# Kernel tuning notes

Hardware: AMD Instinct MI355X
Metric: run time of the kernel (lower is better)

## Reference

```python
import jax, jax.numpy as jnp
import numpy as np

NEG_SLOPE = 0.2

def _gat(x_src, x_dst, W_src, W_dst, a_src, a_dst, bias, src, dst, num_dst):
    # Bipartite PyG GATConv, heads=1, concat, add_self_loops=False.
    h_src = x_src @ W_src              # [N_src, H]
    h_dst = x_dst @ W_dst              # [N_dst, H]
    # Per-edge attention logits: leaky_relu(a_src.h_src[i] + a_dst.h_dst[j])
    e = jax.nn.leaky_relu((h_src @ a_src)[src] + (h_dst @ a_dst)[dst], NEG_SLOPE)  # [E]
    # Segment softmax over incoming edges of each dst node
    m = jax.ops.segment_max(e, dst, num_segments=num_dst)
    m = jnp.where(jnp.isfinite(m), m, 0.0)  # empty segments -> safe
    ex = jnp.exp(e - m[dst])
    denom = jax.ops.segment_sum(ex, dst, num_segments=num_dst)
    alpha = ex / denom[dst]            # [E]
    # Scatter-sum weighted source messages
    out = jax.ops.segment_sum(alpha[:, None] * h_src[src], dst, num_segments=num_dst)
    return out + bias


def setup_inputs() -> dict:
    key = jax.random.key(0)
    ks = jax.random.split(key, 20)
    N_L, N_A, D, H, O, E = 100000, 20000, 128, 128, 64, 500000
    s = 1.0 / np.sqrt(D)
    inp = {
        'x_label': jax.random.normal(ks[0], (N_L, D), jnp.float32),
        'x_attr': jax.random.normal(ks[1], (N_A, D), jnp.float32),
        'W_src_la': jax.random.normal(ks[2], (D, H), jnp.float32) * s,
        'W_dst_la': jax.random.normal(ks[3], (D, H), jnp.float32) * s,
        'a_src_la': jax.random.normal(ks[4], (H,), jnp.float32) * s,
        'a_dst_la': jax.random.normal(ks[5], (H,), jnp.float32) * s,
        'b_la': jax.random.normal(ks[6], (H,), jnp.float32) * 0.01,
        'W_src_al': jax.random.normal(ks[7], (D, H), jnp.float32) * s,
        'W_dst_al': jax.random.normal(ks[8], (D, H), jnp.float32) * s,
        'a_src_al': jax.random.normal(ks[9], (H,), jnp.float32) * s,
        'a_dst_al': jax.random.normal(ks[10], (H,), jnp.float32) * s,
        'b_al': jax.random.normal(ks[11], (H,), jnp.float32) * 0.01,
        'W_lin': jax.random.normal(ks[12], (H, O), jnp.float32) * s,
        'b_lin': jax.random.normal(ks[13], (O,), jnp.float32) * 0.01,
        'edge_src_la': jax.random.randint(ks[14], (E,), 0, N_L, jnp.int32),
        'edge_dst_la': jax.random.randint(ks[15], (E,), 0, N_A, jnp.int32),
        'edge_src_al': jax.random.randint(ks[16], (E,), 0, N_A, jnp.int32),
        'edge_dst_al': jax.random.randint(ks[17], (E,), 0, N_L, jnp.int32),
    }
    return inp


def reference(x_label, x_attr, W_src_la, W_dst_la, a_src_la, a_dst_la, b_la,
              W_src_al, W_dst_al, a_src_al, a_dst_al, b_al, W_lin, b_lin,
              edge_src_la, edge_dst_la, edge_src_al, edge_dst_al):
    N_L = x_label.shape[0]
    N_A = x_attr.shape[0]
    # label -> attribute GAT (output for 'attribute' nodes)
    h_attr = _gat(x_label, x_attr, W_src_la, W_dst_la, a_src_la, a_dst_la, b_la,
                  edge_src_la, edge_dst_la, N_A)
    # attribute -> label GAT (output for 'label' nodes)
    h_label = _gat(x_attr, x_label, W_src_al, W_dst_al, a_src_al, a_dst_al, b_al,
                   edge_src_al, edge_dst_al, N_L)
    h_attr = jax.nn.relu(h_attr)  # computed as in original (unused downstream)
    h_label = jax.nn.relu(h_label)
    out = h_label @ W_lin + b_lin
    return out
```

## Files before the change

kernel.cpp:

```cpp
#include <hip/hip_runtime.h>
#include <math.h>

#define NEG_SLOPE 0.2f

typedef __attribute__((ext_vector_type(8))) short bf16x8;
typedef __attribute__((ext_vector_type(4))) float f32x4;

__device__ __forceinline__ unsigned short f2bf(float f) {
    unsigned u = __float_as_uint(f);
    unsigned r = (u + 0x7FFFu + ((u >> 16) & 1u)) >> 16;
    return (unsigned short)r;
}

__device__ __forceinline__ void acc8(float* a, uint4 u, float x) {
    a[0] += x * __uint_as_float(u.x << 16);
    a[1] += x * __uint_as_float(u.x & 0xFFFF0000u);
    a[2] += x * __uint_as_float(u.y << 16);
    a[3] += x * __uint_as_float(u.y & 0xFFFF0000u);
    a[4] += x * __uint_as_float(u.z << 16);
    a[5] += x * __uint_as_float(u.z & 0xFFFF0000u);
    a[6] += x * __uint_as_float(u.w << 16);
    a[7] += x * __uint_as_float(u.w & 0xFFFF0000u);
}

__global__ void k_wvec(const float* __restrict__ Wd, const float* __restrict__ ad,
                       const float* __restrict__ Ws, const float* __restrict__ as_,
                       float* __restrict__ wdst, float* __restrict__ wsrc) {
    int t = threadIdx.x;
    const float* W = (t < 128) ? Wd : Ws;
    const float* a = (t < 128) ? ad : as_;
    int d = t & 127;
    float s = 0.f;
    #pragma unroll 8
    for (int h = 0; h < 128; ++h) s += W[d * 128 + h] * a[h];
    if (t < 128) wdst[d] = s; else wsrc[d] = s;
}

__global__ void k_rowdot(const float* __restrict__ X, const float* __restrict__ v,
                         float* __restrict__ out, int n) {
    int gw = (int)((blockIdx.x * blockDim.x + threadIdx.x) >> 6);
    int lane = threadIdx.x & 63;
    int half = lane >> 5, li = lane & 31;
    int row = gw * 2 + half;
    if (row >= n) return;
    const float4* X4 = (const float4*)X;
    const float4* V4 = (const float4*)v;
    float4 x = X4[(size_t)row * 32 + li];
    float4 b = V4[li];
    float p = x.x * b.x + x.y * b.y + x.z * b.z + x.w * b.w;
    #pragma unroll
    for (int off = 16; off; off >>= 1) p += __shfl_xor(p, off);
    if (li == 0) out[row] = p;
}

__global__ __launch_bounds__(256) void k_hsrc(const float* __restrict__ X,
                                              const float* __restrict__ W,
                                              unsigned short* __restrict__ Hb, int nrows) {
    __shared__ float Xs[32][128];
    int t = threadIdx.x;
    int row0 = blockIdx.x * 32;
    #pragma unroll
    for (int i = 0; i < 16; ++i) {
        int idx = t + i * 256;
        int r = idx >> 7;
        Xs[r][idx & 127] = (row0 + r < nrows) ? X[(size_t)row0 * 128 + idx] : 0.f;
    }
    __syncthreads();
    int cg = t & 31, rg = t >> 5;
    float acc[4][4];
    #pragma unroll
    for (int i = 0; i < 4; ++i)
        #pragma unroll
        for (int j = 0; j < 4; ++j) acc[i][j] = 0.f;
    const float4* W4 = (const float4*)W;
    #pragma unroll 4
    for (int d = 0; d < 128; ++d) {
        float4 wv = W4[d * 32 + cg];
        float x0 = Xs[rg * 4 + 0][d], x1 = Xs[rg * 4 + 1][d];
        float x2 = Xs[rg * 4 + 2][d], x3 = Xs[rg * 4 + 3][d];
        acc[0][0] += x0 * wv.x; acc[0][1] += x0 * wv.y; acc[0][2] += x0 * wv.z; acc[0][3] += x0 * wv.w;
        acc[1][0] += x1 * wv.x; acc[1][1] += x1 * wv.y; acc[1][2] += x1 * wv.z; acc[1][3] += x1 * wv.w;
        acc[2][0] += x2 * wv.x; acc[2][1] += x2 * wv.y; acc[2][2] += x2 * wv.z; acc[2][3] += x2 * wv.w;
        acc[3][0] += x3 * wv.x; acc[3][1] += x3 * wv.y; acc[3][2] += x3 * wv.z; acc[3][3] += x3 * wv.w;
    }
    #pragma unroll
    for (int i = 0; i < 4; ++i) {
        int gr = row0 + rg * 4 + i;
        if (gr < nrows) {
            ushort4 o;
            o.x = f2bf(acc[i][0]); o.y = f2bf(acc[i][1]);
            o.z = f2bf(acc[i][2]); o.w = f2bf(acc[i][3]);
            *(ushort4*)&Hb[(size_t)gr * 128 + cg * 4] = o;
        }
    }
}

__global__ void k_deg(const int* __restrict__ dst, int* __restrict__ deg, int E) {
    int i = blockIdx.x * blockDim.x + threadIdx.x;
    if (i < E) atomicAdd(&deg[dst[i]], 1);
}

__global__ __launch_bounds__(256) void k_scanA(const int* __restrict__ deg,
                                               int* __restrict__ bsum, int n) {
    __shared__ int sd[256];
    int t = threadIdx.x;
    int base = blockIdx.x * 1024 + t * 4;
    int s = 0;
    #pragma unroll
    for (int i = 0; i < 4; ++i) if (base + i < n) s += deg[base + i];
    sd[t] = s;
    __syncthreads();
    for (int off = 128; off; off >>= 1) {
        if (t < off) sd[t] += sd[t + off];
        __syncthreads();
    }
    if (t == 0) bsum[blockIdx.x] = sd[0];
}

__global__ __launch_bounds__(128) void k_scanB(int* __restrict__ bsum, int nb,
                                               int* __restrict__ rowptr, int n, int E) {
    __shared__ int ss[128];
    int t = threadIdx.x;
    if (nb <= 128) {
        int v = (t < nb) ? bsum[t] : 0;
        ss[t] = v;
        __syncthreads();
        for (int off = 1; off < 128; off <<= 1) {
            int u = (t >= off) ? ss[t - off] : 0;
            __syncthreads();
            ss[t] += u;
            __syncthreads();
        }
        if (t < nb) bsum[t] = ss[t] - v;
    } else if (t == 0) {
        int run = 0;
        for (int i = 0; i < nb; ++i) { int v = bsum[i]; bsum[i] = run; run += v; }
    }
    if (t == 0) rowptr[n] = E;
}

__global__ __launch_bounds__(256) void k_scanC(const int* __restrict__ deg,
                                               const int* __restrict__ bsum,
                                               int* __restrict__ rowptr, int n) {
    __shared__ int ss[256];
    int t = threadIdx.x;
    int base = blockIdx.x * 1024 + t * 4;
    int d[4]; int tsum = 0;
    #pragma unroll
    for (int i = 0; i < 4; ++i) { d[i] = (base + i < n) ? deg[base + i] : 0; tsum += d[i]; }
    ss[t] = tsum;
    __syncthreads();
    for (int off = 1; off < 256; off <<= 1) {
        int v = (t >= off) ? ss[t - off] : 0;
        __syncthreads();
        ss[t] += v;
        __syncthreads();
    }
    int excl = ss[t] - tsum + bsum[blockIdx.x];
    #pragma unroll
    for (int i = 0; i < 4; ++i) {
        if (base + i < n) rowptr[base + i] = excl;
        excl += d[i];
    }
}

__global__ void k_scatter(const int* __restrict__ src, const int* __restrict__ dst,
                          const float* __restrict__ ssrc, const float* __restrict__ sdst,
                          const int* __restrict__ rowptr, int* __restrict__ cursor,
                          int2* __restrict__ csr_pair, int E) {
    int i = blockIdx.x * blockDim.x + threadIdx.x;
    if (i >= E) return;
    int s = src[i], d = dst[i];
    float e = ssrc[s] + sdst[d];
    e = e > 0.f ? e : NEG_SLOPE * e;
    float ex = __expf(e);
    int pos = rowptr[d] + atomicAdd(&cursor[d], 1);
    csr_pair[pos] = make_int2(s, __float_as_int(ex));
}

__global__ __launch_bounds__(256) void k_gat(
    const int* __restrict__ rowptr, const int2* __restrict__ csr_pair,
    const unsigned short* __restrict__ Hb, const float* __restrict__ b_al,
    unsigned short* __restrict__ Gb, int n) {
    int t = threadIdx.x;
    int wave = t >> 6, lane = t & 63;
    int grp = lane >> 4, gl = lane & 15;
    int row = blockIdx.x * 16 + wave * 4 + grp;
    if (row >= n) return;
    int beg = rowptr[row], end = rowptr[row + 1];
    const uint4* H16 = (const uint4*)Hb;
    float a[8];
    #pragma unroll
    for (int k = 0; k < 8; ++k) a[k] = 0.f;
    float denom = 0.f;
    int j = beg;
    for (; j + 4 <= end; j += 4) {
        int2 p0 = csr_pair[j], p1 = csr_pair[j + 1];
        int2 p2 = csr_pair[j + 2], p3 = csr_pair[j + 3];
        float x0 = __int_as_float(p0.y), x1 = __int_as_float(p1.y);
        float x2 = __int_as_float(p2.y), x3 = __int_as_float(p3.y);
        uint4 u0 = H16[(size_t)p0.x * 16 + gl];
        uint4 u1 = H16[(size_t)p1.x * 16 + gl];
        uint4 u2 = H16[(size_t)p2.x * 16 + gl];
        uint4 u3 = H16[(size_t)p3.x * 16 + gl];
        denom += (x0 + x1) + (x2 + x3);
        acc8(a, u0, x0); acc8(a, u1, x1); acc8(a, u2, x2); acc8(a, u3, x3);
    }
    for (; j + 2 <= end; j += 2) {
        int2 p0 = csr_pair[j], p1 = csr_pair[j + 1];
        float x0 = __int_as_float(p0.y), x1 = __int_as_float(p1.y);
        uint4 u0 = H16[(size_t)p0.x * 16 + gl];
        uint4 u1 = H16[(size_t)p1.x * 16 + gl];
        denom += x0 + x1;
        acc8(a, u0, x0); acc8(a, u1, x1);
    }
    if (j < end) {
        int2 p0 = csr_pair[j];
        float x0 = __int_as_float(p0.y);
        uint4 u0 = H16[(size_t)p0.x * 16 + gl];
        denom += x0;
        acc8(a, u0, x0);
    }
    float inv = denom > 0.f ? 1.f / denom : 0.f;
    const float4* B4 = (const float4*)b_al;
    float4 bA = B4[gl * 2], bB = B4[gl * 2 + 1];
    ushort4 ga, gb;
    ga.x = f2bf(fmaxf(a[0] * inv + bA.x, 0.f)); ga.y = f2bf(fmaxf(a[1] * inv + bA.y, 0.f));
    ga.z = f2bf(fmaxf(a[2] * inv + bA.z, 0.f)); ga.w = f2bf(fmaxf(a[3] * inv + bA.w, 0.f));
    gb.x = f2bf(fmaxf(a[4] * inv + bB.x, 0.f)); gb.y = f2bf(fmaxf(a[5] * inv + bB.y, 0.f));
    gb.z = f2bf(fmaxf(a[6] * inv + bB.z, 0.f)); gb.w = f2bf(fmaxf(a[7] * inv + bB.w, 0.f));
    unsigned short* Gr = Gb + (size_t)row * 128 + gl * 8;
    *(ushort4*)Gr = ga;
    *(ushort4*)(Gr + 4) = gb;
}

__global__ void k_wconv(const float* __restrict__ Wlin, unsigned short* __restrict__ Wb) {
    int idx = blockIdx.x * 256 + threadIdx.x;
    int col = idx >> 7, k = idx & 127;
    Wb[idx] = f2bf(Wlin[k * 64 + col]);
}

__global__ __launch_bounds__(256) void k_out_mfma(
    const unsigned short* __restrict__ Gb, const unsigned short* __restrict__ Wb,
    const float* __restrict__ b_lin, float* __restrict__ out, int n) {
    int t = threadIdx.x;
    int wave = t >> 6, lane = t & 63;
    int m = lane & 15, kq = lane >> 4;
    int row0 = blockIdx.x * 64 + wave * 16;
    int ra = row0 + m;
    if (ra >= n) ra = n - 1;
    const bf16x8* A = (const bf16x8*)(Gb + (size_t)ra * 128);
    f32x4 acc0 = {0.f, 0.f, 0.f, 0.f};
    f32x4 acc1 = {0.f, 0.f, 0.f, 0.f};
    f32x4 acc2 = {0.f, 0.f, 0.f, 0.f};
    f32x4 acc3 = {0.f, 0.f, 0.f, 0.f};
    const bf16x8* B0 = (const bf16x8*)(Wb + (size_t)(0 * 16 + m) * 128);
    const bf16x8* B1 = (const bf16x8*)(Wb + (size_t)(1 * 16 + m) * 128);
    const bf16x8* B2 = (const bf16x8*)(Wb + (size_t)(2 * 16 + m) * 128);
    const bf16x8* B3 = (const bf16x8*)(Wb + (size_t)(3 * 16 + m) * 128);
    #pragma unroll
    for (int s = 0; s < 4; ++s) {
        int ci = s * 4 + kq;
        bf16x8 a = A[ci];
        acc0 = __builtin_amdgcn_mfma_f32_16x16x32_bf16(a, B0[ci], acc0, 0, 0, 0);
        acc1 = __builtin_amdgcn_mfma_f32_16x16x32_bf16(a, B1[ci], acc1, 0, 0, 0);
        acc2 = __builtin_amdgcn_mfma_f32_16x16x32_bf16(a, B2[ci], acc2, 0, 0, 0);
        acc3 = __builtin_amdgcn_mfma_f32_16x16x32_bf16(a, B3[ci], acc3, 0, 0, 0);
    }
    float bl0 = b_lin[0 * 16 + m], bl1 = b_lin[1 * 16 + m];
    float bl2 = b_lin[2 * 16 + m], bl3 = b_lin[3 * 16 + m];
    #pragma unroll
    for (int j = 0; j < 4; ++j) {
        int row = row0 + kq * 4 + j;
        if (row < n) {
            float* orow = out + (size_t)row * 64;
            orow[0 * 16 + m] = acc0[j] + bl0;
            orow[1 * 16 + m] = acc1[j] + bl1;
            orow[2 * 16 + m] = acc2[j] + bl2;
            orow[3 * 16 + m] = acc3[j] + bl3;
        }
    }
}

extern "C" void kernel_launch(void* const* d_in, const int* in_sizes, int n_in,
                              void* d_out, int out_size, void* d_ws, size_t ws_size,
                              hipStream_t stream) {
    const float* x_label  = (const float*)d_in[0];
    const float* x_attr   = (const float*)d_in[1];
    const float* W_src_al = (const float*)d_in[7];
    const float* W_dst_al = (const float*)d_in[8];
    const float* a_src_al = (const float*)d_in[9];
    const float* a_dst_al = (const float*)d_in[10];
    const float* b_al     = (const float*)d_in[11];
    const float* W_lin    = (const float*)d_in[12];
    const float* b_lin    = (const float*)d_in[13];
    const int* edge_src   = (const int*)d_in[16];
    const int* edge_dst   = (const int*)d_in[17];

    const int D = 128;
    const int N_L = in_sizes[0] / D;
    const int N_A = in_sizes[1] / D;
    const int E   = in_sizes[16];
    const int nb  = (N_L + 1023) / 1024;

    float* ws = (float*)d_ws;
    float* s_src = ws;
    float* s_dst = s_src + N_A;
    float* wdst  = s_dst + N_L;
    float* wsrc  = wdst + 128;
    int*   deg    = (int*)(wsrc + 128);
    int*   cursor = deg + N_L;
    int*   rowptr = cursor + N_L;
    int*   bsum   = rowptr + N_L + 4;
    int2*  csr_pair = (int2*)(bsum + 128);
    unsigned short* Hb = (unsigned short*)(csr_pair + E);
    unsigned short* Gb = Hb + (size_t)N_A * 128;
    unsigned short* Wb = Gb + (size_t)(N_L + 64) * 128;
    float* out = (float*)d_out;

    hipMemsetAsync(deg, 0, (size_t)2 * N_L * sizeof(int), stream);

    k_wvec<<<1, 256, 0, stream>>>(W_dst_al, a_dst_al, W_src_al, a_src_al, wdst, wsrc);
    k_rowdot<<<(N_L + 7) / 8, 256, 0, stream>>>(x_label, wdst, s_dst, N_L);
    k_rowdot<<<(N_A + 7) / 8, 256, 0, stream>>>(x_attr, wsrc, s_src, N_A);
    k_wconv<<<32, 256, 0, stream>>>(W_lin, Wb);
    k_hsrc<<<(N_A + 31) / 32, 256, 0, stream>>>(x_attr, W_src_al, Hb, N_A);
    k_deg<<<(E + 255) / 256, 256, 0, stream>>>(edge_dst, deg, E);
    k_scanA<<<nb, 256, 0, stream>>>(deg, bsum, N_L);
    k_scanB<<<1, 128, 0, stream>>>(bsum, nb, rowptr, N_L, E);
    k_scanC<<<nb, 256, 0, stream>>>(deg, bsum, rowptr, N_L);
    k_scatter<<<(E + 255) / 256, 256, 0, stream>>>(edge_src, edge_dst, s_src, s_dst,
                                                   rowptr, cursor, csr_pair, E);
    k_gat<<<(N_L + 15) / 16, 256, 0, stream>>>(rowptr, csr_pair, Hb, b_al, Gb, N_L);
    k_out_mfma<<<(N_L + 63) / 64, 256, 0, stream>>>(Gb, Wb, b_lin, out, N_L);
}
```

Measured before the change: 258.5 us.

## Merge independent launches into role-dispatched kernels and fuse GAT with output GEMM

Independent preprocessing steps are packed into two multi-role kernels. The first handles degree counting, the attention weight vectors and the W_lin bf16 conversion. The second handles the block scan, both row-dot products and the H_src projection. The GAT aggregation is fused with the output MFMA GEMM, so aggregated rows are staged in XOR-swizzled shared memory instead of being written to and reread from a global bf16 buffer. This cuts launch count and global traffic, but the fused kernel uses 16KB of LDS per block and has fewer blocks, each processing 4 rows per group serially, which may reduce the latency hiding for the gathers.

```diff
diff --git a/kernel.cpp b/kernel.cpp
--- a/kernel.cpp
+++ b/kernel.cpp
@@ -23,23 +23,41 @@
     a[7] += x * __uint_as_float(u.w & 0xFFFF0000u);
 }
 
-__global__ void k_wvec(const float* __restrict__ Wd, const float* __restrict__ ad,
-                       const float* __restrict__ Ws, const float* __restrict__ as_,
-                       float* __restrict__ wdst, float* __restrict__ wsrc) {
-    int t = threadIdx.x;
-    const float* W = (t < 128) ? Wd : Ws;
-    const float* a = (t < 128) ? ad : as_;
-    int d = t & 127;
-    float s = 0.f;
-    #pragma unroll 8
-    for (int h = 0; h < 128; ++h) s += W[d * 128 + h] * a[h];
-    if (t < 128) wdst[d] = s; else wsrc[d] = s;
-}
-
-__global__ void k_rowdot(const float* __restrict__ X, const float* __restrict__ v,
-                         float* __restrict__ out, int n) {
-    int gw = (int)((blockIdx.x * blockDim.x + threadIdx.x) >> 6);
-    int lane = threadIdx.x & 63;
+__device__ __forceinline__ unsigned pack2(unsigned short lo, unsigned short hi) {
+    return (unsigned)lo | ((unsigned)hi << 16);
+}
+
+__global__ __launch_bounds__(256) void k_pre(
+    const int* __restrict__ dst, int* __restrict__ deg, int E, int nbDeg,
+    const float* __restrict__ Wd, const float* __restrict__ ad,
+    const float* __restrict__ Ws, const float* __restrict__ as_,
+    float* __restrict__ wdst, float* __restrict__ wsrc,
+    const float* __restrict__ Wlin, unsigned short* __restrict__ Wb) {
+    int b = blockIdx.x, t = threadIdx.x;
+    if (b < nbDeg) {
+        int i = b * 256 + t;
+        if (i < E) atomicAdd(&deg[dst[i]], 1);
+    } else if (b == nbDeg) {
+        const float* W = (t < 128) ? Wd : Ws;
+        const float* a = (t < 128) ? ad : as_;
+        int d = t & 127;
+        float s = 0.f;
+        #pragma unroll 8
+        for (int h = 0; h < 128; ++h) s += W[d * 128 + h] * a[h];
+        if (t < 128) wdst[d] = s; else wsrc[d] = s;
+    } else {
+        int idx = (b - nbDeg - 1) * 256 + t;
+        int col = idx >> 7, k = idx & 127;
+        Wb[idx] = f2bf(Wlin[k * 64 + col]);
+    }
+}
+
+__device__ __forceinline__ void rowdot_role(const float* __restrict__ X,
+                                            const float* __restrict__ v,
+                                            float* __restrict__ out, int n,
+                                            int vb, int t) {
+    int gw = vb * 4 + (t >> 6);
+    int lane = t & 63;
     int half = lane >> 5, li = lane & 31;
     int row = gw * 2 + half;
     if (row >= n) return;
@@ -53,17 +71,16 @@
     if (li == 0) out[row] = p;
 }
 
-__global__ __launch_bounds__(256) void k_hsrc(const float* __restrict__ X,
-                                              const float* __restrict__ W,
-                                              unsigned short* __restrict__ Hb, int nrows) {
-    __shared__ float Xs[32][128];
-    int t = threadIdx.x;
-    int row0 = blockIdx.x * 32;
+__device__ __forceinline__ void hsrc_role(const float* __restrict__ X,
+                                          const float* __restrict__ W,
+                                          unsigned short* __restrict__ Hb,
+                                          int nrows, int row0, int t,
+                                          float* __restrict__ Xs ) {
     #pragma unroll
     for (int i = 0; i < 16; ++i) {
         int idx = t + i * 256;
         int r = idx >> 7;
-        Xs[r][idx & 127] = (row0 + r < nrows) ? X[(size_t)row0 * 128 + idx] : 0.f;
+        Xs[r * 128 + (idx & 127)] = (row0 + r < nrows) ? X[(size_t)row0 * 128 + idx] : 0.f;
     }
     __syncthreads();
     int cg = t & 31, rg = t >> 5;
@@ -76,8 +93,8 @@
     #pragma unroll 4
     for (int d = 0; d < 128; ++d) {
         float4 wv = W4[d * 32 + cg];
-        float x0 = Xs[rg * 4 + 0][d], x1 = Xs[rg * 4 + 1][d];
-        float x2 = Xs[rg * 4 + 2][d], x3 = Xs[rg * 4 + 3][d];
+        float x0 = Xs[(rg * 4 + 0) * 128 + d], x1 = Xs[(rg * 4 + 1) * 128 + d];
+        float x2 = Xs[(rg * 4 + 2) * 128 + d], x3 = Xs[(rg * 4 + 3) * 128 + d];
         acc[0][0] += x0 * wv.x; acc[0][1] += x0 * wv.y; acc[0][2] += x0 * wv.z; acc[0][3] += x0 * wv.w;
         acc[1][0] += x1 * wv.x; acc[1][1] += x1 * wv.y; acc[1][2] += x1 * wv.z; acc[1][3] += x1 * wv.w;
         acc[2][0] += x2 * wv.x; acc[2][1] += x2 * wv.y; acc[2][2] += x2 * wv.z; acc[2][3] += x2 * wv.w;
@@ -95,26 +112,35 @@
     }
 }
 
-__global__ void k_deg(const int* __restrict__ dst, int* __restrict__ deg, int E) {
-    int i = blockIdx.x * blockDim.x + threadIdx.x;
-    if (i < E) atomicAdd(&deg[dst[i]], 1);
-}
-
-__global__ __launch_bounds__(256) void k_scanA(const int* __restrict__ deg,
-                                               int* __restrict__ bsum, int n) {
-    __shared__ int sd[256];
-    int t = threadIdx.x;
-    int base = blockIdx.x * 1024 + t * 4;
-    int s = 0;
-    #pragma unroll
-    for (int i = 0; i < 4; ++i) if (base + i < n) s += deg[base + i];
-    sd[t] = s;
-    __syncthreads();
-    for (int off = 128; off; off >>= 1) {
-        if (t < off) sd[t] += sd[t + off];
+__global__ __launch_bounds__(256) void k_mid(
+    const int* __restrict__ deg, int* __restrict__ bsum, int nScan, int n,
+    const float* __restrict__ xL, const float* __restrict__ wdst,
+    float* __restrict__ sdst, int nRL, int NL,
+    const float* __restrict__ xA, const float* __restrict__ wsrc,
+    float* __restrict__ ssrc, int nRA, int NA,
+    const float* __restrict__ Wsrc, unsigned short* __restrict__ Hb) {
+    __shared__ float smemf[32 * 128];
+    int b = blockIdx.x, t = threadIdx.x;
+    if (b < nScan) {
+        int* sd = (int*)smemf;
+        int base = b * 1024 + t * 4;
+        int s = 0;
+        #pragma unroll
+        for (int i = 0; i < 4; ++i) if (base + i < n) s += deg[base + i];
+        sd[t] = s;
         __syncthreads();
-    }
-    if (t == 0) bsum[blockIdx.x] = sd[0];
+        for (int off = 128; off; off >>= 1) {
+            if (t < off) sd[t] += sd[t + off];
+            __syncthreads();
+        }
+        if (t == 0) bsum[b] = sd[0];
+    } else if (b < nScan + nRL) {
+        rowdot_role(xL, wdst, sdst, NL, b - nScan, t);
+    } else if (b < nScan + nRL + nRA) {
+        rowdot_role(xA, wsrc, ssrc, NA, b - nScan - nRL, t);
+    } else {
+        hsrc_role(xA, Wsrc, Hb, NA, (b - nScan - nRL - nRA) * 32, t, smemf);
+    }
 }
 
 __global__ __launch_bounds__(128) void k_scanB(int* __restrict__ bsum, int nb,
@@ -178,78 +204,77 @@
     csr_pair[pos] = make_int2(s, __float_as_int(ex));
 }
 
-__global__ __launch_bounds__(256) void k_gat(
+__global__ __launch_bounds__(256) void k_gatout(
     const int* __restrict__ rowptr, const int2* __restrict__ csr_pair,
     const unsigned short* __restrict__ Hb, const float* __restrict__ b_al,
-    unsigned short* __restrict__ Gb, int n) {
+    const unsigned short* __restrict__ Wb, const float* __restrict__ b_lin,
+    float* __restrict__ out, int n) {
+    __shared__ unsigned short Gs[64 * 128];
     int t = threadIdx.x;
     int wave = t >> 6, lane = t & 63;
     int grp = lane >> 4, gl = lane & 15;
-    int row = blockIdx.x * 16 + wave * 4 + grp;
-    if (row >= n) return;
-    int beg = rowptr[row], end = rowptr[row + 1];
     const uint4* H16 = (const uint4*)Hb;
-    float a[8];
-    #pragma unroll
-    for (int k = 0; k < 8; ++k) a[k] = 0.f;
-    float denom = 0.f;
-    int j = beg;
-    for (; j + 4 <= end; j += 4) {
-        int2 p0 = csr_pair[j], p1 = csr_pair[j + 1];
-        int2 p2 = csr_pair[j + 2], p3 = csr_pair[j + 3];
-        float x0 = __int_as_float(p0.y), x1 = __int_as_float(p1.y);
-        float x2 = __int_as_float(p2.y), x3 = __int_as_float(p3.y);
-        uint4 u0 = H16[(size_t)p0.x * 16 + gl];
-        uint4 u1 = H16[(size_t)p1.x * 16 + gl];
-        uint4 u2 = H16[(size_t)p2.x * 16 + gl];
-        uint4 u3 = H16[(size_t)p3.x * 16 + gl];
-        denom += (x0 + x1) + (x2 + x3);
-        acc8(a, u0, x0); acc8(a, u1, x1); acc8(a, u2, x2); acc8(a, u3, x3);
-    }
-    for (; j + 2 <= end; j += 2) {
-        int2 p0 = csr_pair[j], p1 = csr_pair[j + 1];
-        float x0 = __int_as_float(p0.y), x1 = __int_as_float(p1.y);
-        uint4 u0 = H16[(size_t)p0.x * 16 + gl];
-        uint4 u1 = H16[(size_t)p1.x * 16 + gl];
-        denom += x0 + x1;
-        acc8(a, u0, x0); acc8(a, u1, x1);
-    }
-    if (j < end) {
-        int2 p0 = csr_pair[j];
-        float x0 = __int_as_float(p0.y);
-        uint4 u0 = H16[(size_t)p0.x * 16 + gl];
-        denom += x0;
-        acc8(a, u0, x0);
-    }
-    float inv = denom > 0.f ? 1.f / denom : 0.f;
+    int row0b = blockIdx.x * 64;
     const float4* B4 = (const float4*)b_al;
     float4 bA = B4[gl * 2], bB = B4[gl * 2 + 1];
-    ushort4 ga, gb;
-    ga.x = f2bf(fmaxf(a[0] * inv + bA.x, 0.f)); ga.y = f2bf(fmaxf(a[1] * inv + bA.y, 0.f));
-    ga.z = f2bf(fmaxf(a[2] * inv + bA.z, 0.f)); ga.w = f2bf(fmaxf(a[3] * inv + bA.w, 0.f));
-    gb.x = f2bf(fmaxf(a[4] * inv + bB.x, 0.f)); gb.y = f2bf(fmaxf(a[5] * inv + bB.y, 0.f));
-    gb.z = f2bf(fmaxf(a[6] * inv + bB.z, 0.f)); gb.w = f2bf(fmaxf(a[7] * inv + bB.w, 0.f));
-    unsigned short* Gr = Gb + (size_t)row * 128 + gl * 8;
-    *(ushort4*)Gr = ga;
-    *(ushort4*)(Gr + 4) = gb;
-}
-
-__global__ void k_wconv(const float* __restrict__ Wlin, unsigned short* __restrict__ Wb) {
-    int idx = blockIdx.x * 256 + threadIdx.x;
-    int col = idx >> 7, k = idx & 127;
-    Wb[idx] = f2bf(Wlin[k * 64 + col]);
-}
-
-__global__ __launch_bounds__(256) void k_out_mfma(
-    const unsigned short* __restrict__ Gb, const unsigned short* __restrict__ Wb,
-    const float* __restrict__ b_lin, float* __restrict__ out, int n) {
-    int t = threadIdx.x;
-    int wave = t >> 6, lane = t & 63;
+
+    #pragma unroll
+    for (int rr = 0; rr < 4; ++rr) {
+        int rl = wave * 16 + rr * 4 + grp;
+        int row = row0b + rl;
+        uint4 gpack = make_uint4(0u, 0u, 0u, 0u);
+        if (row < n) {
+            int beg = rowptr[row], end = rowptr[row + 1];
+            float a[8];
+            #pragma unroll
+            for (int k = 0; k < 8; ++k) a[k] = 0.f;
+            float denom = 0.f;
+            int j = beg;
+            for (; j + 4 <= end; j += 4) {
+                int2 p0 = csr_pair[j], p1 = csr_pair[j + 1];
+                int2 p2 = csr_pair[j + 2], p3 = csr_pair[j + 3];
+                float x0 = __int_as_float(p0.y), x1 = __int_as_float(p1.y);
+                float x2 = __int_as_float(p2.y), x3 = __int_as_float(p3.y);
+                uint4 u0 = H16[(size_t)p0.x * 16 + gl];
+                uint4 u1 = H16[(size_t)p1.x * 16 + gl];
+                uint4 u2 = H16[(size_t)p2.x * 16 + gl];
+                uint4 u3 = H16[(size_t)p3.x * 16 + gl];
+                denom += (x0 + x1) + (x2 + x3);
+                acc8(a, u0, x0); acc8(a, u1, x1); acc8(a, u2, x2); acc8(a, u3, x3);
+            }
+            for (; j + 2 <= end; j += 2) {
+                int2 p0 = csr_pair[j], p1 = csr_pair[j + 1];
+                float x0 = __int_as_float(p0.y), x1 = __int_as_float(p1.y);
+                uint4 u0 = H16[(size_t)p0.x * 16 + gl];
+                uint4 u1 = H16[(size_t)p1.x * 16 + gl];
+                denom += x0 + x1;
+                acc8(a, u0, x0); acc8(a, u1, x1);
+            }
+            if (j < end) {
+                int2 p0 = csr_pair[j];
+                float x0 = __int_as_float(p0.y);
+                uint4 u0 = H16[(size_t)p0.x * 16 + gl];
+                denom += x0;
+                acc8(a, u0, x0);
+            }
+            float inv = denom > 0.f ? 1.f / denom : 0.f;
+            unsigned short g0 = f2bf(fmaxf(a[0] * inv + bA.x, 0.f));
+            unsigned short g1 = f2bf(fmaxf(a[1] * inv + bA.y, 0.f));
+            unsigned short g2 = f2bf(fmaxf(a[2] * inv + bA.z, 0.f));
+            unsigned short g3 = f2bf(fmaxf(a[3] * inv + bA.w, 0.f));
+            unsigned short g4 = f2bf(fmaxf(a[4] * inv + bB.x, 0.f));
+            unsigned short g5 = f2bf(fmaxf(a[5] * inv + bB.y, 0.f));
+            unsigned short g6 = f2bf(fmaxf(a[6] * inv + bB.z, 0.f));
+            unsigned short g7 = f2bf(fmaxf(a[7] * inv + bB.w, 0.f));
+            gpack = make_uint4(pack2(g0, g1), pack2(g2, g3), pack2(g4, g5), pack2(g6, g7));
+        }
+        int slot = gl ^ (rl & 15);
+        *(uint4*)&Gs[rl * 128 + slot * 8] = gpack;
+    }
+    __syncthreads();
+
     int m = lane & 15, kq = lane >> 4;
-    int row0 = blockIdx.x * 64 + wave * 16;
-    int ra = row0 + m;
-    if (ra >= n) ra = n - 1;
-    const bf16x8* A = (const bf16x8*)(Gb + (size_t)ra * 128);
+    int rl = wave * 16 + m;
     f32x4 acc0 = {0.f, 0.f, 0.f, 0.f};
     f32x4 acc1 = {0.f, 0.f, 0.f, 0.f};
     f32x4 acc2 = {0.f, 0.f, 0.f, 0.f};
@@ -261,7 +286,8 @@
     #pragma unroll
     for (int s = 0; s < 4; ++s) {
         int ci = s * 4 + kq;
-        bf16x8 a = A[ci];
+        int slot = ci ^ m;
+        bf16x8 a = *(const bf16x8*)&Gs[rl * 128 + slot * 8];
         acc0 = __builtin_amdgcn_mfma_f32_16x16x32_bf16(a, B0[ci], acc0, 0, 0, 0);
         acc1 = __builtin_amdgcn_mfma_f32_16x16x32_bf16(a, B1[ci], acc1, 0, 0, 0);
         acc2 = __builtin_amdgcn_mfma_f32_16x16x32_bf16(a, B2[ci], acc2, 0, 0, 0);
@@ -269,6 +295,7 @@
     }
     float bl0 = b_lin[0 * 16 + m], bl1 = b_lin[1 * 16 + m];
     float bl2 = b_lin[2 * 16 + m], bl3 = b_lin[3 * 16 + m];
+    int row0 = row0b + wave * 16;
     #pragma unroll
     for (int j = 0; j < 4; ++j) {
         int row = row0 + kq * 4 + j;
@@ -301,7 +328,12 @@
     const int N_L = in_sizes[0] / D;
     const int N_A = in_sizes[1] / D;
     const int E   = in_sizes[16];
-    const int nb  = (N_L + 1023) / 1024;
+
+    const int nbDeg = (E + 255) / 256;
+    const int nScan = (N_L + 1023) / 1024;
+    const int nRL   = (N_L + 7) / 8;
+    const int nRA   = (N_A + 7) / 8;
+    const int nH    = (N_A + 31) / 32;
 
     float* ws = (float*)d_ws;
     float* s_src = ws;
@@ -310,27 +342,28 @@
     float* wsrc  = wdst + 128;
     int*   deg    = (int*)(wsrc + 128);
     int*   cursor = deg + N_L;
-    int*   rowptr = cursor + N_L;
-    int*   bsum   = rowptr + N_L + 4;
-    int2*  csr_pair = (int2*)(bsum + 128);
+    int*   bsum   = cursor + N_L;
+    int*   rowptr = bsum + 128;
+    int2*  csr_pair = (int2*)(rowptr + N_L + 4);
     unsigned short* Hb = (unsigned short*)(csr_pair + E);
-    unsigned short* Gb = Hb + (size_t)N_A * 128;
-    unsigned short* Wb = Gb + (size_t)(N_L + 64) * 128;
+    unsigned short* Wb = Hb + (size_t)N_A * 128;
+
     float* out = (float*)d_out;
 
     hipMemsetAsync(deg, 0, (size_t)2 * N_L * sizeof(int), stream);
 
-    k_wvec<<<1, 256, 0, stream>>>(W_dst_al, a_dst_al, W_src_al, a_src_al, wdst, wsrc);
-    k_rowdot<<<(N_L + 7) / 8, 256, 0, stream>>>(x_label, wdst, s_dst, N_L);
-    k_rowdot<<<(N_A + 7) / 8, 256, 0, stream>>>(x_attr, wsrc, s_src, N_A);
-    k_wconv<<<32, 256, 0, stream>>>(W_lin, Wb);
-    k_hsrc<<<(N_A + 31) / 32, 256, 0, stream>>>(x_attr, W_src_al, Hb, N_A);
-    k_deg<<<(E + 255) / 256, 256, 0, stream>>>(edge_dst, deg, E);
-    k_scanA<<<nb, 256, 0, stream>>>(deg, bsum, N_L);
-    k_scanB<<<1, 128, 0, stream>>>(bsum, nb, rowptr, N_L, E);
-    k_scanC<<<nb, 256, 0, stream>>>(deg, bsum, rowptr, N_L);
-    k_scatter<<<(E + 255) / 256, 256, 0, stream>>>(edge_src, edge_dst, s_src, s_dst,
-                                                   rowptr, cursor, csr_pair, E);
-    k_gat<<<(N_L + 15) / 16, 256, 0, stream>>>(rowptr, csr_pair, Hb, b_al, Gb, N_L);
-    k_out_mfma<<<(N_L + 63) / 64, 256, 0, stream>>>(Gb, Wb, b_lin, out, N_L);
-}
+    k_pre<<<nbDeg + 1 + 32, 256, 0, stream>>>(edge_dst, deg, E, nbDeg,
+                                              W_dst_al, a_dst_al, W_src_al, a_src_al,
+                                              wdst, wsrc, W_lin, Wb);
+    k_mid<<<nScan + nRL + nRA + nH, 256, 0, stream>>>(
+        deg, bsum, nScan, N_L,
+        x_label, wdst, s_dst, nRL, N_L,
+        x_attr, wsrc, s_src, nRA, N_A,
+        W_src_al, Hb);
+    k_scanB<<<1, 128, 0, stream>>>(bsum, nScan, rowptr, N_L, E);
+    k_scanC<<<nScan, 256, 0, stream>>>(deg, bsum, rowptr, N_L);
+    k_scatter<<<nbDeg, 256, 0, stream>>>(edge_src, edge_dst, s_src, s_dst,
+                                         rowptr, cursor, csr_pair, E);
+    k_gatout<<<(N_L + 63) / 64, 256, 0, stream>>>(rowptr, csr_pair, Hb, b_al,
+                                                  Wb, b_lin, out, N_L);
+}
```

Result: no change. 257.5 us (-0.4%).
